# Optimization experiments

Measured on AMD Instinct MI355X. Metric: run time of the kernel, lower is better.

Reference implementation:

```python
import jax, jax.numpy as jnp
import numpy as np

# ---- P4M (D4) group: 8 elements, idx = 4*m + r (m: mirror bit, r: rot90 count) ----
G = 8

def _mr(i):
    return i // 4, i % 4

def _gidx(m, r):
    return 4 * (m % 2) + (r % 4)

def _comp(a, b):
    m1, r1 = _mr(a); m2, r2 = _mr(b)
    return _gidx(m1 + m2, (r1 if m2 == 0 else -r1) + r2)

_INV = [next(b for b in range(G) if _comp(a, b) == 0) for a in range(G)]
# _PERM[h, g] = index of h^{-1} * g  (left regular action on the group axis)
_PERM = np.array([[_comp(_INV[h], g) for g in range(G)] for h in range(G)])


def _spatial_transform(K, h):
    # act on the last two (spatial) kernel axes by group element h = mirror^m rot^r
    m, r = _mr(h)
    if m:
        K = jnp.flip(K, axis=-1)
    return jnp.rot90(K, k=r, axes=(-2, -1))


def _transformed_kernels(W):
    # W: [N_out, N_in, G, k, k] -> [G, N_out, N_in, G, k, k], one kernel per output group element
    return jnp.stack([_spatial_transform(W[:, :, _PERM[h]], h) for h in range(G)])


def conv_gg(x, W, padding):
    # group->group convolution. x: [B, N_in, G, H, W]; W: [N_out, N_in, G, k, k]
    B, Ni, _, H, Wd = x.shape
    No, k = W.shape[0], W.shape[-1]
    K = _transformed_kernels(W).reshape(G * No, Ni * G, k, k)
    y = jax.lax.conv_general_dilated(
        x.reshape(B, Ni * G, H, Wd), K, window_strides=(1, 1),
        padding=[(padding, padding), (padding, padding)],
        dimension_numbers=('NCHW', 'OIHW', 'NCHW'))
    Ho, Wo = y.shape[-2], y.shape[-1]
    return y.reshape(B, G, No, Ho, Wo).transpose(0, 2, 1, 3, 4)  # [B, N_out, G, Ho, Wo]


def channel_att_gg(x, W1, W2):
    # squeeze-excite over (channel, group) with group-equivariant weight sharing
    s = x.mean(axis=(-2, -1))                                  # [B, C, G]
    P1 = W1[:, :, _PERM]                                       # [M, C, G_out, G_in]
    t = jax.nn.relu(jnp.einsum('mcog,bcg->bmo', P1, s))        # [B, M, G]
    P2 = W2[:, :, _PERM]                                       # [C, M, G_out, G_in]
    return jax.nn.sigmoid(jnp.einsum('cmog,bmg->bco', P2, t))  # [B, C, G]


def spatial_att_gg(x, Wsp):
    # CBAM-style: mean/max over channels, group-equivariant 7x7 conv, sigmoid
    p = jnp.stack([x.mean(axis=1), x.max(axis=1)], axis=1)     # [B, 2, G, H, W]
    return jax.nn.sigmoid(conv_gg(p, Wsp, padding=Wsp.shape[-1] // 2))  # [B, 1, G, H, W]


def f_att_conv_gg(x, W, Wc1, Wc2, Wsp, padding):
    a_ch = channel_att_gg(x, Wc1, Wc2)[:, :, :, None, None]
    a_sp = spatial_att_gg(x, Wsp)
    return conv_gg(x * a_ch * a_sp, W, padding)


def bn3d(x, gamma, beta, eps=2e-5):
    # training-mode BatchNorm3d: stats over (B, G, H, W) per channel, biased variance
    mu = x.mean(axis=(0, 2, 3, 4), keepdims=True)
    var = ((x - mu) ** 2).mean(axis=(0, 2, 3, 4), keepdims=True)
    return (x - mu) * jax.lax.rsqrt(var + eps) * gamma[None, :, None, None, None] \
        + beta[None, :, None, None, None]


C, MID, K, SPK, B, H = 96, 48, 3, 7, 4, 56  # MID = C // ratio-reduction (ratio = C//2)


def setup_inputs() -> dict:
    key = jax.random.key(0)
    ks = jax.random.split(key, 12)
    def rn(k, shape, scale):
        return jax.random.normal(k, shape, dtype=jnp.float32) * scale
    wsc = float(np.sqrt(2.0 / (C * G * K * K)))
    asc = float(np.sqrt(2.0 / (C * G)))
    ssc = float(np.sqrt(2.0 / (2 * G * SPK * SPK)))
    return {
        'x': rn(ks[0], (B, C, G, H, H), 1.0),
        'bn1_gamma': jnp.ones((C,), jnp.float32), 'bn1_beta': jnp.zeros((C,), jnp.float32),
        'bn2_gamma': jnp.ones((C,), jnp.float32), 'bn2_beta': jnp.zeros((C,), jnp.float32),
        'c1_W': rn(ks[1], (C, C, G, K, K), wsc),
        'c1_att1': rn(ks[2], (MID, C, G), asc), 'c1_att2': rn(ks[3], (C, MID, G), asc),
        'c1_sp': rn(ks[4], (1, 2, G, SPK, SPK), ssc),
        'c2_W': rn(ks[5], (C, C, G, K, K), wsc),
        'c2_att1': rn(ks[6], (MID, C, G), asc), 'c2_att2': rn(ks[7], (C, MID, G), asc),
        'c2_sp': rn(ks[8], (1, 2, G, SPK, SPK), ssc),
    }


def reference(x, bn1_gamma, bn1_beta, bn2_gamma, bn2_beta,
              c1_W, c1_att1, c1_att2, c1_sp,
              c2_W, c2_att1, c2_att2, c2_sp):
    # fiber_map='id', stride=1 -> no group pooling, identity shortcut
    h = f_att_conv_gg(jax.nn.relu(bn3d(x, bn1_gamma, bn1_beta)),
                      c1_W, c1_att1, c1_att2, c1_sp, padding=1)
    h = f_att_conv_gg(jax.nn.relu(bn3d(h, bn2_gamma, bn2_beta)),
                      c2_W, c2_att1, c2_att2, c2_sp, padding=1)
    return x + h
```

## Files before the change

kernel.cpp:

```cpp
#include <hip/hip_runtime.h>
#include <math.h>

#define NG 8
#define C96 96
#define NMID 48
#define HW 56
#define PIX 3136
#define GHW 25088
#define CIN 768
#define NPIXT 9633792
#define BN_N 100352
#define PADW 58
#define PADPIX 3364
#define WTK 589824
#define PPL 3968
#define WBASE 16384

typedef __attribute__((ext_vector_type(8))) short bf16x8;
typedef __attribute__((ext_vector_type(4))) float f32x4;

__device__ __forceinline__ int d_comp(int a, int b){
  int m1=a>>2, r1=a&3, m2=b>>2, r2=b&3;
  int m=(m1+m2)&1;
  int r = (m2==0) ? (r1+r2) : (r2-r1);
  r = (r+4)&3;
  return 4*m+r;
}
__device__ __forceinline__ int d_inv(int a){ return (a>>2) ? a : ((4-(a&3))&3); }
__device__ __forceinline__ int d_perm(int h, int g){ return d_comp(d_inv(h), g); }

__device__ __forceinline__ void d_src(int h, int dy, int dx, int n, int* sy, int* sx){
  int r=h&3, m=h>>2, e=n-1;
  int y,x;
  if(r==0){y=dy; x=dx;}
  else if(r==1){y=dx; x=e-dy;}
  else if(r==2){y=e-dy; x=e-dx;}
  else {y=e-dx; x=dy;}
  if(m) x = e-x;
  *sy=y; *sx=x;
}

__device__ __forceinline__ unsigned short f2bf(float f){
  unsigned int u = __builtin_bit_cast(unsigned int, f);
  unsigned int r = (u + 0x7FFFu + ((u>>16)&1u)) >> 16;
  return (unsigned short)r;
}

__device__ __forceinline__ void gload_lds16(const void* g, void* l){
  __builtin_amdgcn_global_load_lds((const __attribute__((address_space(1))) unsigned int*)g,
                                   (__attribute__((address_space(3))) unsigned int*)l, 16, 0, 0);
}

#define VMCNT0() asm volatile("s_waitcnt vmcnt(0)" ::: "memory")
#define BAR() do { __builtin_amdgcn_s_barrier(); __builtin_amdgcn_sched_barrier(0); } while(0)

__global__ void k_bn_stats(const float* __restrict__ in, float* __restrict__ spart){
  __shared__ float sm[8];
  int c = blockIdx.x, s = blockIdx.y;
  int b = s>>1, half = s&1;
  const float4* p = (const float4*)(in + ((size_t)(b*C96 + c))*GHW) + half*(GHW/8);
  float sum=0.f, sum2=0.f;
  for (int i=threadIdx.x; i<GHW/8; i+=256){
    float4 v = p[i];
    sum  += v.x+v.y+v.z+v.w;
    sum2 += v.x*v.x+v.y*v.y+v.z*v.z+v.w*v.w;
  }
  #pragma unroll
  for (int off=32; off>0; off>>=1){ sum += __shfl_down(sum,off); sum2 += __shfl_down(sum2,off); }
  int lane=threadIdx.x&63, wid=threadIdx.x>>6;
  if(lane==0){ sm[wid]=sum; sm[4+wid]=sum2; }
  __syncthreads();
  if(threadIdx.x==0){
    float a=sm[0]+sm[1]+sm[2]+sm[3], b2=sm[4]+sm[5]+sm[6]+sm[7];
    spart[(c*8+s)*2]   = a;
    spart[(c*8+s)*2+1] = b2;
  }
}

__global__ __launch_bounds__(256) void k_pool(const float* __restrict__ in,
    const float* __restrict__ spart, const float* __restrict__ gamma, const float* __restrict__ beta,
    float* __restrict__ pp){
  __shared__ float scs[C96], shs[C96];
  int tid = threadIdx.x;
  if (tid < C96){
    float s=0.f, s2=0.f;
    #pragma unroll
    for (int k=0;k<8;k++){ s += spart[(tid*8+k)*2]; s2 += spart[(tid*8+k)*2+1]; }
    float mean = s*(1.f/BN_N);
    float var  = s2*(1.f/BN_N) - mean*mean;
    float sc = gamma[tid]*rsqrtf(var + 2e-5f);
    scs[tid] = sc; shs[tid] = beta[tid] - mean*sc;
  }
  __syncthreads();
  int bg = blockIdx.y; int b = bg>>3, g = bg&7;
  int px = blockIdx.x*256 + tid;
  if (px >= PIX) return;
  float pm = 0.f, pmx = 0.f;
  for (int c = 0; c < C96; c++){
    size_t idx = ((size_t)((b*C96 + c)*8 + g))*PIX + px;
    float v = fmaxf(fmaf(in[idx], scs[c], shs[c]), 0.f);
    pm += v; pmx = fmaxf(pmx, v);
  }
  int y = px/HW, x = px - y*HW;
  pp[(size_t)(b*16 + g)*PPL     + (y+3)*64 + (x+3)] = pm;
  pp[(size_t)(b*16 + 8 + g)*PPL + (y+3)*64 + (x+3)] = pmx;
}

__global__ void k_chan(const float* __restrict__ in, const float* __restrict__ spart,
    const float* __restrict__ gamma, const float* __restrict__ beta, float* __restrict__ sout){
  int bcg = blockIdx.x;
  int c = (bcg >> 3) % C96;
  float s=0.f, s2=0.f;
  #pragma unroll
  for (int k=0;k<8;k++){ s += spart[(c*8+k)*2]; s2 += spart[(c*8+k)*2+1]; }
  float mean = s*(1.f/BN_N);
  float var  = s2*(1.f/BN_N) - mean*mean;
  float sc = gamma[c]*rsqrtf(var + 2e-5f);
  float sh = beta[c] - mean*sc;
  const float4* p = (const float4*)(in + (size_t)bcg*PIX);
  float acc=0.f;
  for (int i=threadIdx.x; i<PIX/4; i+=64){
    float4 v = p[i];
    acc += fmaxf(fmaf(v.x,sc,sh),0.f) + fmaxf(fmaf(v.y,sc,sh),0.f)
         + fmaxf(fmaf(v.z,sc,sh),0.f) + fmaxf(fmaf(v.w,sc,sh),0.f);
  }
  #pragma unroll
  for(int off=32;off>0;off>>=1) acc += __shfl_down(acc,off);
  if(threadIdx.x==0) sout[bcg] = acc * (1.f/3136.f);
}

__global__ void k_ca(const float* __restrict__ sbuf, const float* __restrict__ W1,
                     const float* __restrict__ W2, float* __restrict__ ach){
  __shared__ float sl[CIN], tl[NMID*8];
  int b = blockIdx.x, tid = threadIdx.x;
  sl[tid] = sbuf[b*CIN + tid];
  __syncthreads();
  int o = tid & 7;
  int pg[8];
  #pragma unroll
  for (int g=0; g<8; g++) pg[g] = d_perm(o, g);
  if (tid < NMID*8){
    int m = tid >> 3;
    float acc = 0.f;
    for (int c=0; c<C96; c++){
      #pragma unroll
      for (int g=0; g<8; g++) acc += W1[(m*C96+c)*8+pg[g]] * sl[c*8+g];
    }
    tl[tid] = fmaxf(acc, 0.f);
  }
  __syncthreads();
  {
    int c = tid >> 3;
    float acc = 0.f;
    for (int m=0; m<NMID; m++){
      #pragma unroll
      for (int g=0; g<8; g++) acc += W2[(c*NMID+m)*8+pg[g]] * tl[(m<<3)+g];
    }
    ach[b*CIN + tid] = 1.f/(1.f+__expf(-acc));
  }
}

__global__ __launch_bounds__(256) void k_sp_conv(const float* __restrict__ pp,
    const float* __restrict__ Wsp, float* __restrict__ aspt){
  __shared__ float wl[2*8*49];
  int bh = blockIdx.y; int b=bh>>3, h=bh&7;
  for(int idx=threadIdx.x; idx<784; idx+=256){
    int i = idx/392; int rem = idx-i*392;
    int g = rem/49; int kk = rem-g*49;
    int dy=kk/7, dx=kk-dy*7;
    int pg = d_perm(h,g);
    int sy,sx; d_src(h,dy,dx,7,&sy,&sx);
    wl[idx] = Wsp[(i*8+pg)*49 + sy*7+sx] * (i==0 ? (1.f/96.f) : 1.f);
  }
  __syncthreads();
  int pix = blockIdx.x*256 + threadIdx.x;
  if(pix>=PIX) return;
  int y=pix/HW, x=pix-y*HW;
  const float* base = pp + (size_t)(b*16)*PPL + y*64 + x;
  float acc=0.f;
  for(int ig=0; ig<16; ig++){
    const float* pb = base + (size_t)ig*PPL;
    const float* wb = wl + ig*49;
    #pragma unroll
    for(int dy=0; dy<7; dy++){
      #pragma unroll
      for(int dx=0; dx<7; dx++)
        acc = fmaf(pb[dy*64+dx], wb[dy*7+dx], acc);
    }
  }
  aspt[((size_t)b*PIX + pix)*8 + h] = 1.f/(1.f+__expf(-acc));
}

__global__ void k_zero(uint4* __restrict__ xp, uint4* __restrict__ pp){
  size_t i = (size_t)blockIdx.x*256 + threadIdx.x;
  uint4 z = (uint4){0u,0u,0u,0u};
  if (i < 1291392) xp[i] = z;
  else { size_t j = i - 1291392; if (j < 63488) pp[j] = z; }
}

__global__ __launch_bounds__(256) void k_mod_t(const float* __restrict__ in,
    const float* __restrict__ spart, const float* __restrict__ gamma, const float* __restrict__ beta,
    const float* __restrict__ ach, const float* __restrict__ aspt,
    unsigned int* __restrict__ XpU){
  __shared__ float tile[64][65];
  __shared__ float scs8[8], shs8[8];
  int b = blockIdx.z;
  int cg0 = blockIdx.y*64;
  int pix0 = blockIdx.x*64;
  int tid = threadIdx.x;
  if (tid < 8){
    int c = (cg0>>3) + tid;
    float s=0.f, s2=0.f;
    #pragma unroll
    for (int k=0;k<8;k++){ s += spart[(c*8+k)*2]; s2 += spart[(c*8+k)*2+1]; }
    float mean = s*(1.f/BN_N);
    float var  = s2*(1.f/BN_N) - mean*mean;
    float sc = gamma[c]*rsqrtf(var + 2e-5f);
    scs8[tid] = sc; shs8[tid] = beta[c] - mean*sc;
  }
  __syncthreads();
  int lane = tid & 63, w = tid >> 6;
  for (int r = w; r < 64; r += 4){
    int cg = cg0 + r;
    float a1 = ach[b*CIN + cg];
    float raw = in[(size_t)(b*CIN + cg)*PIX + pix0 + lane];
    float v = fmaxf(fmaf(raw, scs8[r>>3], shs8[r>>3]), 0.f);
    tile[r][lane] = v * a1;
  }
  __syncthreads();
  int half = lane >> 5;
  int cgA = (lane & 31)*2;
  #pragma unroll
  for (int it = 0; it < 8; it++){
    int p = it*8 + w*2 + half;
    int pix = pix0 + p;
    int y = pix/HW, x = pix - y*HW;
    float2 a2 = *(const float2*)(aspt + ((size_t)b*PIX + pix)*8 + (cgA&7));
    float vA = tile[cgA][p]   * a2.x;
    float vB = tile[cgA+1][p] * a2.y;
    unsigned int u = (unsigned int)f2bf(vA) | ((unsigned int)f2bf(vB) << 16);
    XpU[(((size_t)b*PADPIX + (y+1)*PADW + (x+1))*CIN + cg0 + cgA) >> 1] = u;
  }
}

__global__ void k_ktb2(const float* __restrict__ W1src, const float* __restrict__ W2src,
                       unsigned short* __restrict__ Wt1, unsigned short* __restrict__ Wt2){
  const float* W = blockIdx.y ? W2src : W1src;
  unsigned short* Wt = blockIdx.y ? Wt2 : Wt1;
  int idx = blockIdx.x*256 + threadIdx.x;
  int ci = idx % CIN;
  int t2 = idx / CIN;
  int co = t2 % CIN;
  int kk = t2 / CIN;
  int h = co/C96, o = co - h*C96;
  int i = ci >> 3, g = ci & 7;
  int dy = kk/3, dx = kk - dy*3;
  int sy, sx; d_src(h, dy, dx, 3, &sy, &sx);
  float v = W[((o*C96 + i)*8 + d_perm(h,g))*9 + sy*3 + sx];
  Wt[idx] = f2bf(v);
}

__global__ __launch_bounds__(256, 2) void k_convmf(const unsigned short* __restrict__ Xp,
    const unsigned short* __restrict__ Wt, const float* __restrict__ resid,
    float* __restrict__ out){
  __shared__ unsigned short lds[40960];
  int tid = threadIdx.x, lane = tid & 63, w = tid >> 6;
  int col = lane & 15, kg = lane >> 4;

  int bid = blockIdx.x;
  int wgid = (bid & 7)*56 + (bid >> 3);
  int m = wgid/112; int rem = wgid - m*112;
  int b = rem/28;  int rp = rem - b*28;
  int y0 = rp*2, co0 = m*192;

  int xgo[8], xds[8];
  #pragma unroll
  for (int t = 0; t < 8; t++){
    int fg = (w*8 + t)*64 + lane;
    int row = fg >> 9;
    int pr  = (fg >> 3) & 63;
    int gi  = fg & 7;
    int sg  = gi ^ (pr & 7);
    xgo[t] = (b*PADPIX + (y0+row)*PADW + pr)*CIN + sg*8;
    xds[t] = (w*8 + t)*512;
  }
  int wgo[6], wofs[6];
  {
    int crow = lane >> 3, gi = lane & 7, sg = gi ^ crow;
    #pragma unroll
    for (int j = 0; j < 6; j++){
      int cb = w*48 + j*8;
      wgo[j]  = (co0 + cb + crow)*CIN + sg*8;
      wofs[j] = cb*64;
    }
  }
  int ab[2][3][2];
  #pragma unroll
  for (int q = 0; q < 2; q++)
    #pragma unroll
    for (int mf = 0; mf < 3; mf++)
      #pragma unroll
      for (int ks = 0; ks < 2; ks++)
        ab[q][mf][ks] = WBASE + q*12288 + (w*48 + mf*16 + col)*64 + ((((ks<<2)|kg) ^ (col&7)) << 3);

  int boff[3][7], boff2[3][7];
  #pragma unroll
  for (int nf=0; nf<7; nf++){
    int q2 = nf*16 + col;
    int qyl = (q2 >= 56) ? 1 : 0;
    int qx = q2 - 56*qyl;
    #pragma unroll
    for (int dx=0; dx<3; dx++){
      int t1 = qx + dx;
      boff[dx][nf]  = (qyl<<12) | (t1<<6) | ((kg ^ (t1&7))<<3);
      boff2[dx][nf] = boff[dx][nf] ^ 32;
    }
  }

  f32x4 acc[3][7];
  #pragma unroll
  for (int mf=0; mf<3; mf++)
    #pragma unroll
    for (int nf=0; nf<7; nf++)
      acc[mf][nf] = (f32x4){0.f,0.f,0.f,0.f};

  #pragma unroll
  for (int j = 0; j < 6; j++) gload_lds16(Wt + wgo[j], &lds[WBASE + wofs[j]]);
  #pragma unroll
  for (int t = 0; t < 8; t++) gload_lds16(Xp + xgo[t], &lds[xds[t]]);
  VMCNT0();
  BAR();

  for (int cc = 0; cc < 6; cc++){
    #pragma unroll
    for (int t = 0; t < 18; t++){
      const int ch = t/9;
      const int kk = t - ch*9;
      const int q  = t & 1;
      const int dyk = kk/3, dxk = kk - dyk*3;
      bf16x8 A00 = *(const bf16x8*)(lds + ab[q][0][0]);
      bf16x8 A01 = *(const bf16x8*)(lds + ab[q][0][1]);
      bf16x8 A10 = *(const bf16x8*)(lds + ab[q][1][0]);
      bf16x8 A11 = *(const bf16x8*)(lds + ab[q][1][1]);
      bf16x8 A20 = *(const bf16x8*)(lds + ab[q][2][0]);
      bf16x8 A21 = *(const bf16x8*)(lds + ab[q][2][1]);
      if (t < 17 || cc < 5){
        const int tn = t + 1;
        const int chn = tn/9;
        const int kk2 = tn - chn*9;
        const unsigned short* wsrc = Wt + (size_t)kk2*WTK + cc*128 + chn*64;
        #pragma unroll
        for (int j = 0; j < 6; j++)
          gload_lds16(wsrc + wgo[j], &lds[WBASE + (q^1)*12288 + wofs[j]]);
      }
      const int dyo = dyk << 12;
      __builtin_amdgcn_s_setprio(1);
      #pragma unroll
      for (int nf = 0; nf < 7; nf++){
        bf16x8 B0 = *(const bf16x8*)(lds + boff[dxk][nf]  + dyo);
        bf16x8 B1 = *(const bf16x8*)(lds + boff2[dxk][nf] + dyo);
        acc[0][nf] = __builtin_amdgcn_mfma_f32_16x16x32_bf16(A00, B0, acc[0][nf], 0,0,0);
        acc[1][nf] = __builtin_amdgcn_mfma_f32_16x16x32_bf16(A10, B0, acc[1][nf], 0,0,0);
        acc[2][nf] = __builtin_amdgcn_mfma_f32_16x16x32_bf16(A20, B0, acc[2][nf], 0,0,0);
        acc[0][nf] = __builtin_amdgcn_mfma_f32_16x16x32_bf16(A01, B1, acc[0][nf], 0,0,0);
        acc[1][nf] = __builtin_amdgcn_mfma_f32_16x16x32_bf16(A11, B1, acc[1][nf], 0,0,0);
        acc[2][nf] = __builtin_amdgcn_mfma_f32_16x16x32_bf16(A21, B1, acc[2][nf], 0,0,0);
      }
      __builtin_amdgcn_s_setprio(0);
      VMCNT0();
      BAR();
      if (t == 8 || (t == 17 && cc < 5)){
        const int next = (t == 8) ? 1 : 2;
        const unsigned short* xsrc = Xp + cc*128 + next*64;
        #pragma unroll
        for (int tt = 0; tt < 8; tt++) gload_lds16(xsrc + xgo[tt], &lds[xds[tt]]);
        VMCNT0();
        BAR();
      }
    }
  }

  #pragma unroll
  for (int mf = 0; mf < 3; mf++){
    int co_b = co0 + w*48 + mf*16;
    int h = co_b/C96;
    int ob = co_b - h*C96 + kg*4;
    #pragma unroll
    for (int nf = 0; nf < 7; nf++){
      int qq = nf*16 + col;
      #pragma unroll
      for (int r = 0; r < 4; r++){
        size_t oi = ((size_t)((b*C96 + ob + r)*8 + h))*PIX + y0*56 + qq;
        float v = acc[mf][nf][r];
        if (resid) v += resid[oi];
        out[oi] = v;
      }
    }
  }
}

static void run_layer(const float* bn_in,
                      const float* a1W, const float* a2W, const float* spW,
                      const float* bng, const float* bnb,
                      const float* resid, float* convout,
                      float* spart, float* sbuf, float* ach, float* ppP, float* aspt,
                      unsigned short* Wt, unsigned short* Xp, hipStream_t stream)
{
  k_bn_stats<<<dim3(C96,8),256,0,stream>>>(bn_in, spart);
  k_pool<<<dim3(13,32),256,0,stream>>>(bn_in, spart, bng, bnb, ppP);
  k_chan<<<4*C96*NG,64,0,stream>>>(bn_in, spart, bng, bnb, sbuf);
  k_ca<<<4,CIN,0,stream>>>(sbuf, a1W, a2W, ach);
  k_sp_conv<<<dim3(13,32),256,0,stream>>>(ppP, spW, aspt);
  k_mod_t<<<dim3(PIX/64, CIN/64, 4),256,0,stream>>>(bn_in, spart, bng, bnb, ach, aspt, (unsigned int*)Xp);
  k_convmf<<<448,256,0,stream>>>(Xp, Wt, resid, convout);
}

extern "C" void kernel_launch(void* const* d_in, const int* in_sizes, int n_in,
                              void* d_out, int out_size, void* d_ws, size_t ws_size,
                              hipStream_t stream) {
  const float* x    = (const float*)d_in[0];
  const float* bn1g = (const float*)d_in[1];
  const float* bn1b = (const float*)d_in[2];
  const float* bn2g = (const float*)d_in[3];
  const float* bn2b = (const float*)d_in[4];
  const float* c1W  = (const float*)d_in[5];
  const float* c1a1 = (const float*)d_in[6];
  const float* c1a2 = (const float*)d_in[7];
  const float* c1sp = (const float*)d_in[8];
  const float* c2W  = (const float*)d_in[9];
  const float* c2a1 = (const float*)d_in[10];
  const float* c2a2 = (const float*)d_in[11];
  const float* c2sp = (const float*)d_in[12];
  float* out = (float*)d_out;
  float* ws  = (float*)d_ws;

  float* bufA = ws;
  unsigned short* Wt1 = (unsigned short*)(bufA + NPIXT);
  unsigned short* Wt2 = Wt1 + 9*CIN*CIN;
  unsigned short* Xp  = Wt2 + 9*CIN*CIN;
  float* spart = (float*)(Xp + (size_t)4*PADPIX*CIN);
  float* sbuf  = spart + 1536;
  float* ach   = sbuf + 4*C96*NG;
  float* ppP   = ach + 4*C96*NG;
  float* aspt  = ppP + 4*16*PPL;

  k_ktb2<<<dim3((9*CIN*CIN)/256, 2),256,0,stream>>>(c1W, c2W, Wt1, Wt2);
  k_zero<<<5293,256,0,stream>>>((uint4*)Xp, (uint4*)ppP);

  run_layer(x, c1a1, c1a2, c1sp, bn1g, bn1b, nullptr, bufA,
            spart, sbuf, ach, ppP, aspt, Wt1, Xp, stream);
  run_layer(bufA, c2a1, c2a2, c2sp, bn2g, bn2b, x, out,
            spart, sbuf, ach, ppP, aspt, Wt2, Xp, stream);
}
```

Measured before the change: 555.9 us.

## Drop per-step barriers in conv main loop and zero only padding borders

The implicit-GEMM conv loop now issues the next weight-tile async LDS load before the current step's MFMAs and waits with vmcnt(6) instead of vmcnt(0). The workgroup barrier after every kernel-tap step is removed, since each wave loads and reads only its own weight rows; barriers remain only around input-tile reloads every 64 channels. The zero-init kernel now clears only the padded border of the input buffer instead of the whole buffer, plus the pooling buffer. This cuts barrier stalls and lets load latency overlap with compute. It relies on per-wave ownership of the weight LDS region and on the interior being fully rewritten by the modulation kernel.

```diff
diff --git a/kernel.cpp b/kernel.cpp
--- a/kernel.cpp
+++ b/kernel.cpp
@@ -14,7 +14,6 @@
 #define PADPIX 3364
 #define WTK 589824
 #define PPL 3968
-#define WBASE 16384
 
 typedef __attribute__((ext_vector_type(8))) short bf16x8;
 typedef __attribute__((ext_vector_type(4))) float f32x4;
@@ -51,7 +50,10 @@
                                    (__attribute__((address_space(3))) unsigned int*)l, 16, 0, 0);
 }
 
-#define VMCNT0() asm volatile("s_waitcnt vmcnt(0)" ::: "memory")
+#define VMCNT6() do { asm volatile("s_waitcnt vmcnt(6)" ::: "memory"); \
+                      __builtin_amdgcn_sched_barrier(0); } while(0)
+#define VMCNT0() do { asm volatile("s_waitcnt vmcnt(0)" ::: "memory"); \
+                      __builtin_amdgcn_sched_barrier(0); } while(0)
 #define BAR() do { __builtin_amdgcn_s_barrier(); __builtin_amdgcn_sched_barrier(0); } while(0)
 
 __global__ void k_bn_stats(const float* __restrict__ in, float* __restrict__ spart){
@@ -191,11 +193,21 @@
   aspt[((size_t)b*PIX + pix)*8 + h] = 1.f/(1.f+__expf(-acc));
 }
 
-__global__ void k_zero(uint4* __restrict__ xp, uint4* __restrict__ pp){
-  size_t i = (size_t)blockIdx.x*256 + threadIdx.x;
+__global__ void k_zerob(uint4* __restrict__ xp, uint4* __restrict__ pp){
   uint4 z = (uint4){0u,0u,0u,0u};
-  if (i < 1291392) xp[i] = z;
-  else { size_t j = i - 1291392; if (j < 63488) pp[j] = z; }
+  int i = blockIdx.x*256 + threadIdx.x;
+  if (blockIdx.x < 248){ pp[i] = z; return; }
+  int r = i - 63488;
+  if (r >= 87552) return;
+  int b = r / 21888;
+  int q = r - b*21888;
+  int p = q / 96, j = q - p*96;
+  int y, x;
+  if (p < 58){ y=0; x=p; }
+  else if (p < 116){ y=57; x=p-58; }
+  else if (p < 172){ y=p-115; x=0; }
+  else { y=p-171; x=57; }
+  xp[(size_t)(b*PADPIX + y*PADW + x)*96 + j] = z;
 }
 
 __global__ __launch_bounds__(256) void k_mod_t(const float* __restrict__ in,
@@ -294,16 +306,14 @@
       wofs[j] = cb*64;
     }
   }
-  int ab[2][3][2];
-  #pragma unroll
-  for (int q = 0; q < 2; q++)
-    #pragma unroll
-    for (int mf = 0; mf < 3; mf++)
-      #pragma unroll
-      for (int ks = 0; ks < 2; ks++)
-        ab[q][mf][ks] = WBASE + q*12288 + (w*48 + mf*16 + col)*64 + ((((ks<<2)|kg) ^ (col&7)) << 3);
-
-  int boff[3][7], boff2[3][7];
+  int aidx[3][2];
+  #pragma unroll
+  for (int mf = 0; mf < 3; mf++)
+    #pragma unroll
+    for (int ks = 0; ks < 2; ks++)
+      aidx[mf][ks] = (w*48 + mf*16 + col)*64 + ((((ks<<2)|kg) ^ (col&7)) << 3);
+
+  int boff[3][7];
   #pragma unroll
   for (int nf=0; nf<7; nf++){
     int q2 = nf*16 + col;
@@ -312,8 +322,7 @@
     #pragma unroll
     for (int dx=0; dx<3; dx++){
       int t1 = qx + dx;
-      boff[dx][nf]  = (qyl<<12) | (t1<<6) | ((kg ^ (t1&7))<<3);
-      boff2[dx][nf] = boff[dx][nf] ^ 32;
+      boff[dx][nf] = (qyl<<12) | (t1<<6) | ((kg ^ (t1&7))<<3);
     }
   }
 
@@ -325,40 +334,43 @@
       acc[mf][nf] = (f32x4){0.f,0.f,0.f,0.f};
 
   #pragma unroll
-  for (int j = 0; j < 6; j++) gload_lds16(Wt + wgo[j], &lds[WBASE + wofs[j]]);
+  for (int j = 0; j < 6; j++) gload_lds16(Wt + wgo[j], &lds[16384 + wofs[j]]);
   #pragma unroll
   for (int t = 0; t < 8; t++) gload_lds16(Xp + xgo[t], &lds[xds[t]]);
   VMCNT0();
   BAR();
 
-  for (int cc = 0; cc < 6; cc++){
-    #pragma unroll
-    for (int t = 0; t < 18; t++){
-      const int ch = t/9;
-      const int kk = t - ch*9;
-      const int q  = t & 1;
-      const int dyk = kk/3, dxk = kk - dyk*3;
-      bf16x8 A00 = *(const bf16x8*)(lds + ab[q][0][0]);
-      bf16x8 A01 = *(const bf16x8*)(lds + ab[q][0][1]);
-      bf16x8 A10 = *(const bf16x8*)(lds + ab[q][1][0]);
-      bf16x8 A11 = *(const bf16x8*)(lds + ab[q][1][1]);
-      bf16x8 A20 = *(const bf16x8*)(lds + ab[q][2][0]);
-      bf16x8 A21 = *(const bf16x8*)(lds + ab[q][2][1]);
-      if (t < 17 || cc < 5){
-        const int tn = t + 1;
-        const int chn = tn/9;
-        const int kk2 = tn - chn*9;
-        const unsigned short* wsrc = Wt + (size_t)kk2*WTK + cc*128 + chn*64;
+  int q = 0;
+  for (int chunk = 0; chunk < 12; chunk++){
+    int ci0 = chunk << 6;
+    #pragma unroll
+    for (int kk = 0; kk < 9; kk++){
+      int s = chunk*9 + kk;
+      if (s <= 106){
+        int kk2 = kk + 1, c2 = chunk;
+        if (kk2 == 9){ kk2 = 0; c2++; }
+        size_t gofs = (size_t)kk2*WTK + (c2 << 6);
+        int dofs = 16384 + (q^1)*12288;
         #pragma unroll
-        for (int j = 0; j < 6; j++)
-          gload_lds16(wsrc + wgo[j], &lds[WBASE + (q^1)*12288 + wofs[j]]);
+        for (int j = 0; j < 6; j++) gload_lds16(Wt + gofs + wgo[j], &lds[dofs + wofs[j]]);
+        VMCNT6();
+      } else {
+        VMCNT0();
       }
+      const unsigned short* Wb = &lds[16384 + q*12288];
+      bf16x8 A00 = *(const bf16x8*)(Wb + aidx[0][0]);
+      bf16x8 A01 = *(const bf16x8*)(Wb + aidx[0][1]);
+      bf16x8 A10 = *(const bf16x8*)(Wb + aidx[1][0]);
+      bf16x8 A11 = *(const bf16x8*)(Wb + aidx[1][1]);
+      bf16x8 A20 = *(const bf16x8*)(Wb + aidx[2][0]);
+      bf16x8 A21 = *(const bf16x8*)(Wb + aidx[2][1]);
+      int dyk = kk/3, dxk = kk - dyk*3;
       const int dyo = dyk << 12;
       __builtin_amdgcn_s_setprio(1);
       #pragma unroll
       for (int nf = 0; nf < 7; nf++){
-        bf16x8 B0 = *(const bf16x8*)(lds + boff[dxk][nf]  + dyo);
-        bf16x8 B1 = *(const bf16x8*)(lds + boff2[dxk][nf] + dyo);
+        bf16x8 B0 = *(const bf16x8*)(lds + boff[dxk][nf] + dyo);
+        bf16x8 B1 = *(const bf16x8*)(lds + ((boff[dxk][nf] + dyo) ^ 32));
         acc[0][nf] = __builtin_amdgcn_mfma_f32_16x16x32_bf16(A00, B0, acc[0][nf], 0,0,0);
         acc[1][nf] = __builtin_amdgcn_mfma_f32_16x16x32_bf16(A10, B0, acc[1][nf], 0,0,0);
         acc[2][nf] = __builtin_amdgcn_mfma_f32_16x16x32_bf16(A20, B0, acc[2][nf], 0,0,0);
@@ -367,13 +379,11 @@
         acc[2][nf] = __builtin_amdgcn_mfma_f32_16x16x32_bf16(A21, B1, acc[2][nf], 0,0,0);
       }
       __builtin_amdgcn_s_setprio(0);
-      VMCNT0();
-      BAR();
-      if (t == 8 || (t == 17 && cc < 5)){
-        const int next = (t == 8) ? 1 : 2;
-        const unsigned short* xsrc = Xp + cc*128 + next*64;
+      q ^= 1;
+      if (kk == 8 && chunk < 11){
+        BAR();
         #pragma unroll
-        for (int tt = 0; tt < 8; tt++) gload_lds16(xsrc + xgo[tt], &lds[xds[tt]]);
+        for (int t = 0; t < 8; t++) gload_lds16(Xp + xgo[t] + ci0 + 64, &lds[xds[t]]);
         VMCNT0();
         BAR();
       }
@@ -445,7 +455,7 @@
   float* aspt  = ppP + 4*16*PPL;
 
   k_ktb2<<<dim3((9*CIN*CIN)/256, 2),256,0,stream>>>(c1W, c2W, Wt1, Wt2);
-  k_zero<<<5293,256,0,stream>>>((uint4*)Xp, (uint4*)ppP);
+  k_zerob<<<590,256,0,stream>>>((uint4*)Xp, (uint4*)ppP);
 
   run_layer(x, c1a1, c1a2, c1sp, bn1g, bn1b, nullptr, bufA,
             spart, sbuf, ach, ppP, aspt, Wt1, Xp, stream);
```

Result: faster. 543.5 us (-2.2%).
